# Kernel optimization log

Measured on AMD Instinct MI355X. Metric: run time of the kernel, lower is better.

Reference implementation:

```python
import jax, jax.numpy as jnp
import numpy as np

NUM_CLASSES = 151  # Visual Genome object classes
PRED_DIM = 51      # predicate distribution channels (50 predicates + bg)


def _conv2d(x, w, pad):
    # x: [B, Cin, H, W], w: [Cout, Cin, kh, kw]
    return jax.lax.conv_general_dilated(
        x, w, window_strides=(1, 1), padding=[(pad, pad), (pad, pad)],
        dimension_numbers=("NCHW", "OIHW", "NCHW"))


def setup_inputs() -> dict:
    key = jax.random.key(0)
    ks = jax.random.split(key, 12)
    B, N, D = 64, 80, 4096
    K = D // 4  # 1024
    s = 0.02
    return {
        "encoder_reps": jax.random.normal(ks[0], (B, N, D), jnp.float32),
        "obj_preds": jax.random.randint(ks[1], (B, N), 0, NUM_CLASSES, jnp.int32),
        "freq_table": jax.random.normal(ks[2], (NUM_CLASSES * NUM_CLASSES, PRED_DIM), jnp.float32),
        "W_comp": jax.random.normal(ks[3], (D, K), jnp.float32) * s,
        "W_ou1": jax.random.normal(ks[4], (K, K), jnp.float32) * s,
        "W_ofc": jax.random.normal(ks[5], (K, K), jnp.float32) * s,
        "W_decomp": jax.random.normal(ks[6], (K, D), jnp.float32) * s,
        "conv1": jax.random.normal(ks[7], (10, PRED_DIM, 3, 3), jnp.float32) * s,
        "conv2": jax.random.normal(ks[8], (5, 10, 3, 3), jnp.float32) * s,
        "conv3": jax.random.normal(ks[9], (1, 5, 1, 1), jnp.float32) * s,
    }


def reference(encoder_reps, obj_preds, freq_table, W_comp, W_ou1, W_ofc,
              W_decomp, conv1, conv2, conv3):
    B, N, D = encoder_reps.shape
    # obj_comp: Linear(D, D//4, bias=False) + ReLU
    comp = jax.nn.relu(jnp.einsum("bnd,dk->bnk", encoder_reps, W_comp))  # [B,N,K]
    # ou1: Linear(K, K, bias=False) + ReLU
    obj_u1 = jax.nn.relu(jnp.einsum("bnk,kj->bnj", comp, W_ou1))          # [B,N,K]
    # pairwise product indices -> freq_bias.index_with_labels (subj*C + obj)
    pair_idx = obj_preds[:, :, None] * NUM_CLASSES + obj_preds[:, None, :]  # [B,N,N]
    rel_u1 = freq_table[pair_idx]                                          # [B,N,N,51]
    # adjacency via small conv stack + sigmoid
    x = jnp.transpose(rel_u1, (0, 3, 1, 2))      # [B,51,N,N]
    x = _conv2d(x, conv1, pad=1)                 # [B,10,N,N]
    x = _conv2d(x, conv2, pad=1)                 # [B,5,N,N]
    x = _conv2d(x, conv3, pad=0)                 # [B,1,N,N]
    adj = jax.nn.sigmoid(x[:, 0])                # [B,N,N]
    # normalized Laplacian: D^-1/2 (A + I) D^-1/2
    A_hat = adj + jnp.eye(N, dtype=adj.dtype)[None]
    d = (jnp.sum(A_hat, axis=2) + 1e-5) ** (-0.5)                          # [B,N]
    L_hat = d[:, :, None] * A_hat * d[:, None, :]                          # [B,N,N]
    ofl_u = jnp.einsum("bnm,bmk->bnk", L_hat, obj_u1)                      # [B,N,K]
    # ofc_u + obj_decomp + residual
    u_m = jax.nn.relu(jnp.einsum("bnk,kj->bnj", ofl_u, W_ofc))
    decomp = jax.nn.relu(jnp.einsum("bnk,kd->bnd", u_m, W_decomp))
    return decomp + encoder_reps
```

## Files before the change

kernel.cpp:

```cpp
#include <hip/hip_runtime.h>
#include <hip/hip_bf16.h>
#include <math.h>

typedef __bf16 bf16x8 __attribute__((ext_vector_type(8)));
typedef float floatx4 __attribute__((ext_vector_type(4)));
typedef float float4v __attribute__((ext_vector_type(4)));
typedef float float2v __attribute__((ext_vector_type(2)));
typedef unsigned short ushortx4 __attribute__((ext_vector_type(4)));
typedef unsigned short ushortx8 __attribute__((ext_vector_type(8)));

__device__ __forceinline__ unsigned short f2bf(float f) {
    unsigned int u = __builtin_bit_cast(unsigned int, f);
    u += 0x7FFFu + ((u >> 16) & 1u);
    return (unsigned short)(u >> 16);
}
__device__ __forceinline__ float bf2f(unsigned short h) {
    unsigned int u = ((unsigned int)h) << 16;
    return __builtin_bit_cast(float, u);
}

__device__ __forceinline__ void gload_lds16(const void* g, void* l) {
    __builtin_amdgcn_global_load_lds(
        (const __attribute__((address_space(1))) unsigned int*)g,
        (__attribute__((address_space(3))) unsigned int*)l, 16, 0, 0);
}

__global__ __launch_bounds__(256) void cast_bf16_kernel(
    const float* __restrict__ in, unsigned short* __restrict__ out, long n8)
{
    long i = (long)blockIdx.x * 256 + threadIdx.x;
    long stride = (long)gridDim.x * 256;
    for (; i < n8; i += stride) {
        float4v a = reinterpret_cast<const float4v*>(in)[2 * i];
        float4v b = reinterpret_cast<const float4v*>(in)[2 * i + 1];
        ushortx8 h;
        #pragma unroll
        for (int q = 0; q < 4; ++q) { h[q] = f2bf(a[q]); h[4 + q] = f2bf(b[q]); }
        reinterpret_cast<ushortx8*>(out)[i] = h;
    }
}

__global__ __launch_bounds__(256) void reduce_relu_kernel(
    const unsigned short* __restrict__ p0, const unsigned short* __restrict__ p1,
    unsigned short* __restrict__ out, long n8)
{
    long i = (long)blockIdx.x * 256 + threadIdx.x;
    long stride = (long)gridDim.x * 256;
    const ushortx8* a0 = reinterpret_cast<const ushortx8*>(p0);
    const ushortx8* a1 = reinterpret_cast<const ushortx8*>(p1);
    for (; i < n8; i += stride) {
        ushortx8 x = a0[i], y = a1[i];
        ushortx8 h;
        #pragma unroll
        for (int q = 0; q < 8; ++q)
            h[q] = f2bf(fmaxf(bf2f(x[q]) + bf2f(y[q]), 0.0f));
        reinterpret_cast<ushortx8*>(out)[i] = h;
    }
}

__global__ __launch_bounds__(256) void prep_kernel(
    const float* __restrict__ w1, const float* __restrict__ w2,
    const float* __restrict__ w3, float* __restrict__ W1e,
    float* __restrict__ w23)
{
    for (int idx = threadIdx.x; idx < 4590; idx += 256) {
        int ci = idx / 90, rem = idx % 90;
        int tap = rem / 10, co = rem % 10;
        int di = tap / 3, dj = tap % 3;
        W1e[idx] = w1[((co * 51 + ci) * 3 + di) * 3 + dj];
    }
    if (threadIdx.x < 90) {
        int tap = threadIdx.x / 10, c10 = threadIdx.x % 10;
        int di = tap / 3, dj = tap % 3;
        float s = 0.f;
        #pragma unroll
        for (int c5 = 0; c5 < 5; ++c5)
            s = fmaf(w3[c5], w2[((c5 * 10 + c10) * 3 + di) * 3 + dj], s);
        w23[threadIdx.x] = s;
    }
}

__global__ __launch_bounds__(256) void fp1_kernel(
    const float* __restrict__ freq, const float* __restrict__ W1e,
    float* __restrict__ Fp1)
{
    __shared__ float W1s[4590];
    for (int idx = threadIdx.x; idx < 4590; idx += 256)
        W1s[idx] = W1e[idx];
    __syncthreads();
    int p = blockIdx.x * 256 + threadIdx.x;
    if (p >= 22801) return;
    float2v acc[45];
    #pragma unroll
    for (int t = 0; t < 45; ++t) { acc[t][0] = 0.f; acc[t][1] = 0.f; }
    const float* fr = freq + (size_t)p * 51;
    for (int ci = 0; ci < 51; ++ci) {
        float v = fr[ci];
        const float2v* wrow = reinterpret_cast<const float2v*>(&W1s[ci * 90]);
        #pragma unroll
        for (int t = 0; t < 45; ++t) {
            float2v w = wrow[t];
            acc[t][0] = fmaf(v, w[0], acc[t][0]);
            acc[t][1] = fmaf(v, w[1], acc[t][1]);
        }
    }
    float2v* out = reinterpret_cast<float2v*>(Fp1 + (size_t)p * 90);
    #pragma unroll
    for (int t = 0; t < 45; ++t) out[t] = acc[t];
}

__global__ __launch_bounds__(320) void gather_kernel(
    const int* __restrict__ preds, const float* __restrict__ Fp1,
    float* __restrict__ h1)
{
    __shared__ int pb[80];
    const int b = blockIdx.y;
    const int tid = threadIdx.x;
    if (tid < 80) pb[tid] = preds[b * 80 + tid];
    __syncthreads();
    const int i = blockIdx.x * 4 + tid / 80;
    const int j = tid % 80;
    float2v acc[5];
    #pragma unroll
    for (int q = 0; q < 5; ++q) { acc[q][0] = 0.f; acc[q][1] = 0.f; }
    #pragma unroll
    for (int di = 0; di < 3; ++di) {
        int ii = i + di - 1;
        if (ii < 0 || ii >= 80) continue;
        int pi = pb[ii] * 151;
        #pragma unroll
        for (int dj = 0; dj < 3; ++dj) {
            int jj = j + dj - 1;
            if (jj < 0 || jj >= 80) continue;
            const float2v* row = reinterpret_cast<const float2v*>(
                Fp1 + (size_t)(pi + pb[jj]) * 90 + (di * 3 + dj) * 10);
            #pragma unroll
            for (int q = 0; q < 5; ++q) {
                float2v v = row[q];
                acc[q][0] += v[0];
                acc[q][1] += v[1];
            }
        }
    }
    float2v* out = reinterpret_cast<float2v*>(
        h1 + ((size_t)b * 6400 + i * 80 + j) * 10);
    #pragma unroll
    for (int q = 0; q < 5; ++q) out[q] = acc[q];
}

__global__ __launch_bounds__(320) void conv23_kernel(
    const float* __restrict__ h1, const float* __restrict__ w23g,
    float* __restrict__ adj)
{
    __shared__ float w23s[90];
    const int tid = threadIdx.x;
    if (tid < 90) w23s[tid] = w23g[tid];
    __syncthreads();
    const int b = blockIdx.y;
    const int i = blockIdx.x * 4 + tid / 80;
    const int j = tid % 80;
    float t = 0.f;
    #pragma unroll
    for (int di = 0; di < 3; ++di) {
        int ii = i + di - 1;
        if (ii < 0 || ii >= 80) continue;
        #pragma unroll
        for (int dj = 0; dj < 3; ++dj) {
            int jj = j + dj - 1;
            if (jj < 0 || jj >= 80) continue;
            const float2v* hp = reinterpret_cast<const float2v*>(
                h1 + ((size_t)b * 6400 + ii * 80 + jj) * 10);
            const float* wp = w23s + (di * 3 + dj) * 10;
            #pragma unroll
            for (int q = 0; q < 5; ++q) {
                float2v v = hp[q];
                t = fmaf(v[0], wp[2 * q], t);
                t = fmaf(v[1], wp[2 * q + 1], t);
            }
        }
    }
    adj[(size_t)b * 6400 + i * 80 + j] = 1.0f / (1.0f + __expf(-t));
}

__global__ __launch_bounds__(128) void degree_kernel(
    const float* __restrict__ adj, float* __restrict__ deg)
{
    int b = blockIdx.x;
    int i = threadIdx.x;
    if (i >= 80) return;
    const float* row = adj + (size_t)b * 6400 + i * 80;
    float s = 1.0f + 1e-5f;
    for (int jj = 0; jj < 80; ++jj) s += row[jj];
    deg[b * 80 + i] = rsqrtf(s);
}

__global__ __launch_bounds__(256) void transpose_cast(
    const float* __restrict__ in, unsigned short* __restrict__ out,
    int R, int C)
{
    __shared__ float t[32][33];
    const int tx = threadIdx.x & 31;
    const int ty = threadIdx.x >> 5;
    const int r0 = blockIdx.y * 32, c0 = blockIdx.x * 32;
    #pragma unroll
    for (int k = 0; k < 4; ++k)
        t[ty + k * 8][tx] = in[(size_t)(r0 + ty + k * 8) * C + c0 + tx];
    __syncthreads();
    #pragma unroll
    for (int k = 0; k < 4; ++k)
        out[(size_t)(c0 + ty + k * 8) * R + r0 + tx] = f2bf(t[tx][ty + k * 8]);
}

template<int MODE>
__global__ __launch_bounds__(256) void gemm8p(
    const unsigned short* __restrict__ Ap, const unsigned short* __restrict__ Bt,
    void* __restrict__ Cp, const unsigned short* __restrict__ Rb,
    unsigned short* __restrict__ P1,
    int M, int N, int lda, int kh)
{
    __shared__ __align__(16) unsigned short SS[24576];
    unsigned short* Al = SS;
    unsigned short* Bl = SS + 12288;

    const int tid  = threadIdx.x;
    const int bm   = blockIdx.x * 128;
    const int bn   = blockIdx.y * 128;
    const int k0   = blockIdx.z * kh;
    const int wave = tid >> 6;
    const int lane = tid & 63;
    const int wm   = (wave >> 1) * 64;
    const int wn   = (wave & 1) * 64;
    const int lr   = lane & 15;
    const int lo   = lane >> 4;
    const int soct = (lo ^ ((lr >> 1) & 3)) * 8;

    floatx4 acc[4][4];
    #pragma unroll
    for (int i = 0; i < 4; ++i)
        #pragma unroll
        for (int j = 0; j < 4; ++j)
            #pragma unroll
            for (int r = 0; r < 4; ++r) acc[i][j][r] = 0.0f;

    auto stageA = [&](int buf, int kq) {
        #pragma unroll
        for (int it = 0; it < 2; ++it) {
            int idx = tid + it * 256;
            int r = idx >> 2, s = idx & 3;
            gload_lds16(
                &Ap[(size_t)(bm + r) * lda + kq + ((s ^ ((r >> 1) & 3)) * 8)],
                &Al[buf * 4096 + idx * 8]);
        }
    };
    auto stageB = [&](int buf, int kq) {
        #pragma unroll
        for (int it = 0; it < 2; ++it) {
            int idx = tid + it * 256;
            int r = idx >> 2, s = idx & 3;
            gload_lds16(
                &Bt[(size_t)(bn + r) * lda + kq + ((s ^ ((r >> 1) & 3)) * 8)],
                &Bl[buf * 4096 + idx * 8]);
        }
    };

    const int nt = kh >> 5;
    stageA(0, k0);
    stageB(0, k0);
    if (nt > 1) stageA(1, k0 + 32);

    for (int t = 0; t < nt; ++t) {
        const int cur = t % 3;
        if (t + 1 < nt) {
            asm volatile("s_waitcnt vmcnt(2)" ::: "memory");
        } else {
            asm volatile("s_waitcnt vmcnt(0)" ::: "memory");
        }
        __builtin_amdgcn_s_barrier();
        __builtin_amdgcn_sched_barrier(0);

        bf16x8 af[4], bf0[2];
        #pragma unroll
        for (int mi = 0; mi < 4; ++mi)
            af[mi] = *reinterpret_cast<const bf16x8*>(
                &Al[cur * 4096 + (wm + mi * 16 + lr) * 32 + soct]);
        #pragma unroll
        for (int ni = 0; ni < 2; ++ni)
            bf0[ni] = *reinterpret_cast<const bf16x8*>(
                &Bl[cur * 4096 + (wn + ni * 16 + lr) * 32 + soct]);
        if (t + 1 < nt) stageB((t + 1) % 3, k0 + ((t + 1) << 5));
        __builtin_amdgcn_sched_barrier(0);
        __builtin_amdgcn_s_barrier();
        __builtin_amdgcn_s_setprio(1);
        #pragma unroll
        for (int mi = 0; mi < 4; ++mi)
            #pragma unroll
            for (int ni = 0; ni < 2; ++ni)
                acc[mi][ni] = __builtin_amdgcn_mfma_f32_16x16x32_bf16(
                    bf0[ni], af[mi], acc[mi][ni], 0, 0, 0);
        __builtin_amdgcn_s_setprio(0);

        bf16x8 bf1[2];
        #pragma unroll
        for (int ni = 0; ni < 2; ++ni)
            bf1[ni] = *reinterpret_cast<const bf16x8*>(
                &Bl[cur * 4096 + (wn + (ni + 2) * 16 + lr) * 32 + soct]);
        if (t + 2 < nt) stageA((t + 2) % 3, k0 + ((t + 2) << 5));
        __builtin_amdgcn_sched_barrier(0);
        __builtin_amdgcn_s_barrier();
        __builtin_amdgcn_s_setprio(1);
        #pragma unroll
        for (int mi = 0; mi < 4; ++mi)
            #pragma unroll
            for (int ni = 0; ni < 2; ++ni)
                acc[mi][ni + 2] = __builtin_amdgcn_mfma_f32_16x16x32_bf16(
                    bf1[ni], af[mi], acc[mi][ni + 2], 0, 0, 0);
        __builtin_amdgcn_s_setprio(0);
    }

    __syncthreads();
    if (MODE == 1) {
        #pragma unroll
        for (int p = 0; p < 2; ++p) {
            if ((wave & 1) == p) {
                #pragma unroll
                for (int mi = 0; mi < 4; ++mi) {
                    const int mrow = wm + mi * 16 + lr;
                    const int swz = (mrow & 7) << 4;
                    #pragma unroll
                    for (int ni = 0; ni < 4; ++ni) {
                        const int nc = ni * 16 + lo * 4;
                        float4v v;
                        #pragma unroll
                        for (int rr = 0; rr < 4; ++rr) v[rr] = acc[mi][ni][rr];
                        *reinterpret_cast<float4v*>(
                            (char*)SS + ((mrow * 256 + nc * 4) ^ swz)) = v;
                    }
                }
            }
            __syncthreads();
            #pragma unroll
            for (int it = 0; it < 8; ++it) {
                int idx = tid + it * 256;
                int r = idx >> 4, c = idx & 15;
                float4v v = *reinterpret_cast<const float4v*>(
                    (char*)SS + ((r * 256 + c * 16) ^ ((r & 7) << 4)));
                size_t off = (size_t)(bm + r) * N + bn + p * 64 + c * 4;
                ushortx4 rv = *reinterpret_cast<const ushortx4*>(&Rb[off]);
                float4v o;
                #pragma unroll
                for (int rr = 0; rr < 4; ++rr)
                    o[rr] = fmaxf(v[rr], 0.f) + bf2f(rv[rr]);
                *reinterpret_cast<float4v*>(&((float*)Cp)[off]) = o;
            }
            if (p == 0) __syncthreads();
        }
    } else {
        #pragma unroll
        for (int mi = 0; mi < 4; ++mi) {
            const int mrow = wm + mi * 16 + lr;
            const int swz = (mrow & 7) << 4;
            #pragma unroll
            for (int ni = 0; ni < 4; ++ni) {
                const int nc = wn + ni * 16 + lo * 4;
                ushortx4 v;
                #pragma unroll
                for (int rr = 0; rr < 4; ++rr)
                    v[rr] = f2bf(fmaxf(acc[mi][ni][rr], 0.f));
                *reinterpret_cast<ushortx4*>(
                    (char*)SS + ((mrow * 256 + nc * 2) ^ swz)) = v;
            }
        }
        __syncthreads();
        unsigned short* dst = (unsigned short*)Cp;
        #pragma unroll
        for (int it = 0; it < 8; ++it) {
            int idx = tid + it * 256;
            int r = idx >> 4, c = idx & 15;
            ushortx8 v = *reinterpret_cast<const ushortx8*>(
                (char*)SS + ((r * 256 + c * 16) ^ ((r & 7) << 4)));
            *reinterpret_cast<ushortx8*>(
                &dst[(size_t)(bm + r) * N + bn + c * 8]) = v;
        }
    }
}

template<int MODE>
__global__ __launch_bounds__(256) void gemm128(
    const unsigned short* __restrict__ Ap, const unsigned short* __restrict__ Bt,
    void* __restrict__ Cp, const unsigned short* __restrict__ Rb,
    unsigned short* __restrict__ P1,
    int M, int N, int lda, int kh)
{
    __shared__ __align__(16) unsigned short SS[16384];
    unsigned short* Al = SS;
    unsigned short* Bl = SS + 8192;

    const int tid  = threadIdx.x;
    const int bm   = blockIdx.x * 128;
    const int bn   = blockIdx.y * 128;
    const int k0   = blockIdx.z * kh;
    const int wave = tid >> 6;
    const int lane = tid & 63;
    const int wm   = (wave >> 1) * 64;
    const int wn   = (wave & 1) * 64;
    const int lr   = lane & 15;
    const int lo   = lane >> 4;
    const int soct = (lo ^ ((lr >> 1) & 3)) * 8;

    floatx4 acc[4][4];
    #pragma unroll
    for (int i = 0; i < 4; ++i)
        #pragma unroll
        for (int j = 0; j < 4; ++j)
            #pragma unroll
            for (int r = 0; r < 4; ++r) acc[i][j][r] = 0.0f;

    auto stage = [&](int buf, int kq) {
        #pragma unroll
        for (int it = 0; it < 2; ++it) {
            int idx = tid + it * 256;
            int r = idx >> 2, s = idx & 3;
            gload_lds16(
                &Ap[(size_t)(bm + r) * lda + kq + ((s ^ ((r >> 1) & 3)) * 8)],
                &Al[buf * 4096 + idx * 8]);
        }
        #pragma unroll
        for (int it = 0; it < 2; ++it) {
            int idx = tid + it * 256;
            int r = idx >> 2, s = idx & 3;
            gload_lds16(
                &Bt[(size_t)(bn + r) * lda + kq + ((s ^ ((r >> 1) & 3)) * 8)],
                &Bl[buf * 4096 + idx * 8]);
        }
    };

    stage(0, k0);
    __syncthreads();
    const int nt = kh >> 5;
    int cur = 0;
    for (int t = 0; t < nt; ++t) {
        if (t + 1 < nt) stage(cur ^ 1, k0 + ((t + 1) << 5));
        bf16x8 af[4], bfv[4];
        #pragma unroll
        for (int mi = 0; mi < 4; ++mi)
            af[mi] = *reinterpret_cast<const bf16x8*>(
                &Al[cur * 4096 + (wm + mi * 16 + lr) * 32 + soct]);
        #pragma unroll
        for (int ni = 0; ni < 4; ++ni)
            bfv[ni] = *reinterpret_cast<const bf16x8*>(
                &Bl[cur * 4096 + (wn + ni * 16 + lr) * 32 + soct]);
        #pragma unroll
        for (int mi = 0; mi < 4; ++mi)
            #pragma unroll
            for (int ni = 0; ni < 4; ++ni)
                acc[mi][ni] = __builtin_amdgcn_mfma_f32_16x16x32_bf16(
                    bfv[ni], af[mi], acc[mi][ni], 0, 0, 0);
        __syncthreads();
        cur ^= 1;
    }

    #pragma unroll
    for (int mi = 0; mi < 4; ++mi) {
        const int mrow = wm + mi * 16 + lr;
        const int swz = (mrow & 7) << 4;
        #pragma unroll
        for (int ni = 0; ni < 4; ++ni) {
            const int nc = wn + ni * 16 + lo * 4;
            ushortx4 v;
            #pragma unroll
            for (int rr = 0; rr < 4; ++rr)
                v[rr] = f2bf(MODE == 0 ? fmaxf(acc[mi][ni][rr], 0.f)
                                       : acc[mi][ni][rr]);
            *reinterpret_cast<ushortx4*>(
                (char*)SS + ((mrow * 256 + nc * 2) ^ swz)) = v;
        }
    }
    __syncthreads();
    unsigned short* dst = (MODE == 2 && blockIdx.z)
        ? P1 : (unsigned short*)Cp;
    #pragma unroll
    for (int it = 0; it < 8; ++it) {
        int idx = tid + it * 256;
        int r = idx >> 4, c = idx & 15;
        ushortx8 v = *reinterpret_cast<const ushortx8*>(
            (char*)SS + ((r * 256 + c * 16) ^ ((r & 7) << 4)));
        *reinterpret_cast<ushortx8*>(
            &dst[(size_t)(bm + r) * N + bn + c * 8]) = v;
    }
}

__global__ __launch_bounds__(256) void gemm_f32a(
    const float* __restrict__ Ap, const unsigned short* __restrict__ Bt,
    unsigned short* __restrict__ Cp, int M, int N, int lda)
{
    __shared__ unsigned short Al[2][128 * 40];
    __shared__ unsigned short Bl[2][128 * 32];
    const int tid  = threadIdx.x;
    const int bm   = blockIdx.x * 128;
    const int bn   = blockIdx.y * 128;
    const int wave = tid >> 6;
    const int lane = tid & 63;
    const int wm   = (wave >> 1) * 64;
    const int wn   = (wave & 1) * 64;
    const int lr   = lane & 15;
    const int lk   = (lane >> 4) * 8;
    floatx4 acc[4][4];
    #pragma unroll
    for (int i = 0; i < 4; ++i)
        #pragma unroll
        for (int j = 0; j < 4; ++j)
            #pragma unroll
            for (int r = 0; r < 4; ++r) acc[i][j][r] = 0.0f;
    auto stage = [&](int buf, int k0) {
        #pragma unroll
        for (int it = 0; it < 4; ++it) {
            int idx = tid + it * 256;
            int r = idx >> 3, kc = (idx & 7) * 4;
            float4v v = *reinterpret_cast<const float4v*>(
                &Ap[(size_t)(bm + r) * lda + k0 + kc]);
            ushortx4 h;
            #pragma unroll
            for (int q = 0; q < 4; ++q) h[q] = f2bf(v[q]);
            *reinterpret_cast<ushortx4*>(&Al[buf][r * 40 + kc]) = h;
        }
        #pragma unroll
        for (int it = 0; it < 2; ++it) {
            int idx = tid + it * 256;
            gload_lds16(&Bt[(size_t)(bn + (idx >> 2)) * lda + k0 + (idx & 3) * 8],
                        &Bl[buf][idx * 8]);
        }
    };
    stage(0, 0);
    __syncthreads();
    const int nt = lda >> 5;
    int cur = 0;
    for (int t = 0; t < nt; ++t) {
        if (t + 1 < nt) stage(cur ^ 1, (t + 1) << 5);
        bf16x8 af[4], bfv[4];
        #pragma unroll
        for (int mi = 0; mi < 4; ++mi)
            af[mi] = *reinterpret_cast<const bf16x8*>(
                &Al[cur][(wm + mi * 16 + lr) * 40 + lk]);
        #pragma unroll
        for (int ni = 0; ni < 4; ++ni)
            bfv[ni] = *reinterpret_cast<const bf16x8*>(
                &Bl[cur][(wn + ni * 16 + lr) * 32 + lk]);
        #pragma unroll
        for (int mi = 0; mi < 4; ++mi)
            #pragma unroll
            for (int ni = 0; ni < 4; ++ni)
                acc[mi][ni] = __builtin_amdgcn_mfma_f32_16x16x32_bf16(
                    af[mi], bfv[ni], acc[mi][ni], 0, 0, 0);
        __syncthreads();
        cur ^= 1;
    }
    #pragma unroll
    for (int mi = 0; mi < 4; ++mi)
        #pragma unroll
        for (int ni = 0; ni < 4; ++ni)
            #pragma unroll
            for (int r = 0; r < 4; ++r) {
                int row = bm + wm + mi * 16 + (lane >> 4) * 4 + r;
                int col = bn + wn + ni * 16 + lr;
                Cp[(size_t)row * N + col] = f2bf(fmaxf(acc[mi][ni][r], 0.f));
            }
}

__global__ __launch_bounds__(256) void gemm_res_f32(
    const unsigned short* __restrict__ Ap, const unsigned short* __restrict__ Bt,
    float* __restrict__ Cp, const float* __restrict__ Rp, int M, int N, int lda)
{
    __shared__ unsigned short Al[2][128 * 32];
    __shared__ unsigned short Bl[2][128 * 32];
    const int tid  = threadIdx.x;
    const int bm   = blockIdx.x * 128;
    const int bn   = blockIdx.y * 128;
    const int wave = tid >> 6;
    const int lane = tid & 63;
    const int wm   = (wave >> 1) * 64;
    const int wn   = (wave & 1) * 64;
    const int lr   = lane & 15;
    const int lk   = (lane >> 4) * 8;
    floatx4 acc[4][4];
    #pragma unroll
    for (int i = 0; i < 4; ++i)
        #pragma unroll
        for (int j = 0; j < 4; ++j)
            #pragma unroll
            for (int r = 0; r < 4; ++r) acc[i][j][r] = 0.0f;
    auto stage = [&](int buf, int kq) {
        #pragma unroll
        for (int it = 0; it < 2; ++it) {
            int idx = tid + it * 256;
            gload_lds16(&Ap[(size_t)(bm + (idx >> 2)) * lda + kq + (idx & 3) * 8],
                        &Al[buf][idx * 8]);
        }
        #pragma unroll
        for (int it = 0; it < 2; ++it) {
            int idx = tid + it * 256;
            gload_lds16(&Bt[(size_t)(bn + (idx >> 2)) * lda + kq + (idx & 3) * 8],
                        &Bl[buf][idx * 8]);
        }
    };
    stage(0, 0);
    __syncthreads();
    const int nt = lda >> 5;
    int cur = 0;
    for (int t = 0; t < nt; ++t) {
        if (t + 1 < nt) stage(cur ^ 1, (t + 1) << 5);
        bf16x8 af[4], bfv[4];
        #pragma unroll
        for (int mi = 0; mi < 4; ++mi)
            af[mi] = *reinterpret_cast<const bf16x8*>(
                &Al[cur][(wm + mi * 16 + lr) * 32 + lk]);
        #pragma unroll
        for (int ni = 0; ni < 4; ++ni)
            bfv[ni] = *reinterpret_cast<const bf16x8*>(
                &Bl[cur][(wn + ni * 16 + lr) * 32 + lk]);
        #pragma unroll
        for (int mi = 0; mi < 4; ++mi)
            #pragma unroll
            for (int ni = 0; ni < 4; ++ni)
                acc[mi][ni] = __builtin_amdgcn_mfma_f32_16x16x32_bf16(
                    af[mi], bfv[ni], acc[mi][ni], 0, 0, 0);
        __syncthreads();
        cur ^= 1;
    }
    #pragma unroll
    for (int mi = 0; mi < 4; ++mi)
        #pragma unroll
        for (int ni = 0; ni < 4; ++ni)
            #pragma unroll
            for (int r = 0; r < 4; ++r) {
                int row = bm + wm + mi * 16 + (lane >> 4) * 4 + r;
                int col = bn + wn + ni * 16 + lr;
                size_t off = (size_t)row * N + col;
                Cp[off] = fmaxf(acc[mi][ni][r], 0.f) + Rp[off];
            }
}

__global__ __launch_bounds__(256) void laplacian_kernel(
    const float* __restrict__ adj, const float* __restrict__ deg,
    const unsigned short* __restrict__ u_in, unsigned short* __restrict__ ofl)
{
    __shared__ float wl[6400];
    __shared__ unsigned short ul[80 * 256];
    const int b   = blockIdx.y;
    const int kq  = blockIdx.x;
    const int tid = threadIdx.x;
    const int ko  = tid & 31;
    const int ngrp = tid >> 5;

    const float* ab = adj + (size_t)b * 6400;
    const float* db = deg + b * 80;
    for (int idx = tid; idx < 6400; idx += 256) {
        int n = idx / 80;
        int m = idx - n * 80;
        float w = ab[idx] + (n == m ? 1.0f : 0.0f);
        wl[idx] = w * db[m];
    }
    const unsigned short* ub = u_in + (size_t)b * 80 * 1024 + kq * 256;
    #pragma unroll
    for (int it = 0; it < 10; ++it) {
        int idx = tid + it * 256;
        int m   = idx >> 5;
        int c8  = (idx & 31) * 8;
        *reinterpret_cast<ushortx8*>(&ul[m * 256 + c8]) =
            *reinterpret_cast<const ushortx8*>(&ub[(size_t)m * 1024 + c8]);
    }
    __syncthreads();

    float acc[10][8];
    #pragma unroll
    for (int ni = 0; ni < 10; ++ni)
        #pragma unroll
        for (int q = 0; q < 8; ++q) acc[ni][q] = 0.0f;

    for (int m = 0; m < 80; ++m) {
        ushortx8 uv = *reinterpret_cast<const ushortx8*>(&ul[m * 256 + ko * 8]);
        float uf[8];
        #pragma unroll
        for (int q = 0; q < 8; ++q) uf[q] = bf2f(uv[q]);
        #pragma unroll
        for (int ni = 0; ni < 10; ++ni) {
            float wv = wl[(ngrp * 10 + ni) * 80 + m];
            #pragma unroll
            for (int q = 0; q < 8; ++q)
                acc[ni][q] = fmaf(wv, uf[q], acc[ni][q]);
        }
    }
    #pragma unroll
    for (int ni = 0; ni < 10; ++ni) {
        int n = ngrp * 10 + ni;
        float dn = db[n];
        ushortx8 o;
        #pragma unroll
        for (int q = 0; q < 8; ++q) o[q] = f2bf(acc[ni][q] * dn);
        *reinterpret_cast<ushortx8*>(
            &ofl[((size_t)(b * 80 + n)) * 1024 + kq * 256 + ko * 8]) = o;
    }
}

extern "C" void kernel_launch(void* const* d_in, const int* in_sizes, int n_in,
                              void* d_out, int out_size, void* d_ws, size_t ws_size,
                              hipStream_t stream)
{
    const float* enc   = (const float*)d_in[0];
    const int*   preds = (const int*)d_in[1];
    const float* freq  = (const float*)d_in[2];
    const float* Wc    = (const float*)d_in[3];
    const float* Wou1  = (const float*)d_in[4];
    const float* Wofc  = (const float*)d_in[5];
    const float* Wdec  = (const float*)d_in[6];
    const float* w1    = (const float*)d_in[7];
    const float* w2    = (const float*)d_in[8];
    const float* w3    = (const float*)d_in[9];

    const int M = 5120;
    const size_t SLAB = (size_t)M * 1024;
    unsigned short* comp  = (unsigned short*)d_ws;
    unsigned short* obju  = comp + SLAB;
    unsigned short* r1    = obju + SLAB;
    unsigned short* oflu  = r1;
    float*          h1    = (float*)r1;
    unsigned short* r2    = r1 + 8192000;
    unsigned short* um    = r2;
    float*          Fp1   = (float*)r2;
    unsigned short* Wcb   = r2 + SLAB;
    unsigned short* Wou1b = Wcb + (size_t)1024 * 4096;
    unsigned short* Wofcb = Wou1b + (size_t)1024 * 1024;
    unsigned short* Wdecb = Wofcb + (size_t)1024 * 1024;
    float*          W1e   = (float*)(Wdecb + (size_t)4096 * 1024);
    float*          w23   = W1e + 4590;
    float*          adj   = w23 + 90;
    float*          deg   = adj + (size_t)64 * 6400;
    unsigned short* encb  = (unsigned short*)(deg + 5120);
    const size_t need_bytes =
        ((size_t)(encb - comp) + (size_t)M * 4096) * sizeof(unsigned short);
    const bool use_encb = ws_size >= need_bytes;

    prep_kernel<<<1, 256, 0, stream>>>(w1, w2, w3, W1e, w23);
    transpose_cast<<<dim3(32, 128), 256, 0, stream>>>(Wc, Wcb, 4096, 1024);
    transpose_cast<<<dim3(32, 32), 256, 0, stream>>>(Wou1, Wou1b, 1024, 1024);
    transpose_cast<<<dim3(32, 32), 256, 0, stream>>>(Wofc, Wofcb, 1024, 1024);
    transpose_cast<<<dim3(128, 32), 256, 0, stream>>>(Wdec, Wdecb, 1024, 4096);

    fp1_kernel<<<90, 256, 0, stream>>>(freq, W1e, Fp1);
    gather_kernel<<<dim3(20, 64), 320, 0, stream>>>(preds, Fp1, h1);
    conv23_kernel<<<dim3(20, 64), 320, 0, stream>>>(h1, w23, adj);
    degree_kernel<<<64, 128, 0, stream>>>(adj, deg);

    if (use_encb) {
        cast_bf16_kernel<<<2048, 256, 0, stream>>>(enc, encb, (long)M * 4096 / 8);
        gemm128<2><<<dim3(40, 8, 2), 256, 0, stream>>>(
            encb, Wcb, r1, nullptr, r2, M, 1024, 4096, 2048);
        reduce_relu_kernel<<<2048, 256, 0, stream>>>(r1, r2, comp, SLAB / 8);
        gemm128<0><<<dim3(40, 8, 1), 256, 0, stream>>>(
            comp, Wou1b, obju, nullptr, nullptr, M, 1024, 1024, 1024);
    } else {
        gemm_f32a<<<dim3(40, 8), 256, 0, stream>>>(enc, Wcb, comp, M, 1024, 4096);
        gemm128<0><<<dim3(40, 8, 1), 256, 0, stream>>>(
            comp, Wou1b, obju, nullptr, nullptr, M, 1024, 1024, 1024);
    }
    laplacian_kernel<<<dim3(4, 64), 256, 0, stream>>>(adj, deg, obju, oflu);
    if (use_encb) {
        gemm128<0><<<dim3(40, 8, 1), 256, 0, stream>>>(
            oflu, Wofcb, um, nullptr, nullptr, M, 1024, 1024, 1024);
        gemm8p<1><<<dim3(40, 32, 1), 256, 0, stream>>>(
            um, Wdecb, d_out, encb, nullptr, M, 4096, 1024, 1024);
    } else {
        gemm128<0><<<dim3(40, 8, 1), 256, 0, stream>>>(
            oflu, Wofcb, um, nullptr, nullptr, M, 1024, 1024, 1024);
        gemm_res_f32<<<dim3(40, 32), 256, 0, stream>>>(
            um, Wdecb, (float*)d_out, enc, M, 4096, 1024);
    }
}
```

Baseline: 315.0 us.

## Use 64-row GEMM tiles, drop split-K, fuse degree into conv and merge transposes

The 128x128 split-K GEMM for the compression layer and its reduce_relu pass are replaced by a new 64x128-tile GEMM with a fused ReLU epilogue. The same kernel now handles the K=1024 layers, launching 640 blocks instead of 320 to fill more CUs. The four weight transpose launches become one kernel, and the row-degree computation moves into the conv23 kernel, which removes launches and a re-read of adj. In exchange, smaller tiles give less operand reuse per block, and the compression GEMM loses its split-K parallelism over the 4096-long reduction.

```diff
diff --git a/kernel.cpp b/kernel.cpp
--- a/kernel.cpp
+++ b/kernel.cpp
@@ -40,24 +40,6 @@
     }
 }
 
-__global__ __launch_bounds__(256) void reduce_relu_kernel(
-    const unsigned short* __restrict__ p0, const unsigned short* __restrict__ p1,
-    unsigned short* __restrict__ out, long n8)
-{
-    long i = (long)blockIdx.x * 256 + threadIdx.x;
-    long stride = (long)gridDim.x * 256;
-    const ushortx8* a0 = reinterpret_cast<const ushortx8*>(p0);
-    const ushortx8* a1 = reinterpret_cast<const ushortx8*>(p1);
-    for (; i < n8; i += stride) {
-        ushortx8 x = a0[i], y = a1[i];
-        ushortx8 h;
-        #pragma unroll
-        for (int q = 0; q < 8; ++q)
-            h[q] = f2bf(fmaxf(bf2f(x[q]) + bf2f(y[q]), 0.0f));
-        reinterpret_cast<ushortx8*>(out)[i] = h;
-    }
-}
-
 __global__ __launch_bounds__(256) void prep_kernel(
     const float* __restrict__ w1, const float* __restrict__ w2,
     const float* __restrict__ w3, float* __restrict__ W1e,
@@ -80,6 +62,35 @@
     }
 }
 
+__global__ __launch_bounds__(256) void transpose_all(
+    const float* __restrict__ Wc, const float* __restrict__ Wou1,
+    const float* __restrict__ Wofc, const float* __restrict__ Wdec,
+    unsigned short* __restrict__ Wcb, unsigned short* __restrict__ Wou1b,
+    unsigned short* __restrict__ Wofcb, unsigned short* __restrict__ Wdecb)
+{
+    __shared__ float t[32][33];
+    int id = blockIdx.x;
+    const float* in; unsigned short* out; int R, C, bx, by;
+    if (id < 4096)      { in = Wc;   out = Wcb;   R = 4096; C = 1024;
+                          bx = id & 31;  by = id >> 5; }
+    else if (id < 5120) { id -= 4096; in = Wou1; out = Wou1b; R = 1024; C = 1024;
+                          bx = id & 31;  by = id >> 5; }
+    else if (id < 6144) { id -= 5120; in = Wofc; out = Wofcb; R = 1024; C = 1024;
+                          bx = id & 31;  by = id >> 5; }
+    else                { id -= 6144; in = Wdec; out = Wdecb; R = 1024; C = 4096;
+                          bx = id & 127; by = id >> 7; }
+    const int tx = threadIdx.x & 31;
+    const int ty = threadIdx.x >> 5;
+    const int r0 = by * 32, c0 = bx * 32;
+    #pragma unroll
+    for (int k = 0; k < 4; ++k)
+        t[ty + k * 8][tx] = in[(size_t)(r0 + ty + k * 8) * C + c0 + tx];
+    __syncthreads();
+    #pragma unroll
+    for (int k = 0; k < 4; ++k)
+        out[(size_t)(c0 + ty + k * 8) * R + r0 + tx] = f2bf(t[tx][ty + k * 8]);
+}
+
 __global__ __launch_bounds__(256) void fp1_kernel(
     const float* __restrict__ freq, const float* __restrict__ W1e,
     float* __restrict__ Fp1)
@@ -148,11 +159,12 @@
     for (int q = 0; q < 5; ++q) out[q] = acc[q];
 }
 
-__global__ __launch_bounds__(320) void conv23_kernel(
+__global__ __launch_bounds__(320) void conv23_deg_kernel(
     const float* __restrict__ h1, const float* __restrict__ w23g,
-    float* __restrict__ adj)
+    float* __restrict__ adj, float* __restrict__ deg)
 {
     __shared__ float w23s[90];
+    __shared__ float rowv[320];
     const int tid = threadIdx.x;
     if (tid < 90) w23s[tid] = w23g[tid];
     __syncthreads();
@@ -179,36 +191,112 @@
             }
         }
     }
-    adj[(size_t)b * 6400 + i * 80 + j] = 1.0f / (1.0f + __expf(-t));
-}
-
-__global__ __launch_bounds__(128) void degree_kernel(
-    const float* __restrict__ adj, float* __restrict__ deg)
-{
-    int b = blockIdx.x;
-    int i = threadIdx.x;
-    if (i >= 80) return;
-    const float* row = adj + (size_t)b * 6400 + i * 80;
-    float s = 1.0f + 1e-5f;
-    for (int jj = 0; jj < 80; ++jj) s += row[jj];
-    deg[b * 80 + i] = rsqrtf(s);
-}
-
-__global__ __launch_bounds__(256) void transpose_cast(
-    const float* __restrict__ in, unsigned short* __restrict__ out,
-    int R, int C)
-{
-    __shared__ float t[32][33];
-    const int tx = threadIdx.x & 31;
-    const int ty = threadIdx.x >> 5;
-    const int r0 = blockIdx.y * 32, c0 = blockIdx.x * 32;
-    #pragma unroll
-    for (int k = 0; k < 4; ++k)
-        t[ty + k * 8][tx] = in[(size_t)(r0 + ty + k * 8) * C + c0 + tx];
-    __syncthreads();
-    #pragma unroll
-    for (int k = 0; k < 4; ++k)
-        out[(size_t)(c0 + ty + k * 8) * R + r0 + tx] = f2bf(t[tx][ty + k * 8]);
+    float sig = 1.0f / (1.0f + __expf(-t));
+    adj[(size_t)b * 6400 + i * 80 + j] = sig;
+    rowv[tid] = sig;
+    __syncthreads();
+    if (tid < 4) {
+        float s = 1.0f + 1e-5f;
+        #pragma unroll 16
+        for (int jj = 0; jj < 80; ++jj) s += rowv[tid * 80 + jj];
+        deg[b * 80 + blockIdx.x * 4 + tid] = rsqrtf(s);
+    }
+}
+
+__global__ __launch_bounds__(256) void gemm64(
+    const unsigned short* __restrict__ Ap, const unsigned short* __restrict__ Bt,
+    unsigned short* __restrict__ Cp, int M, int N, int lda)
+{
+    __shared__ __align__(16) unsigned short SS[12288];
+    unsigned short* Al = SS;
+    unsigned short* Bl = SS + 4096;
+
+    const int tid  = threadIdx.x;
+    const int bm   = blockIdx.x * 64;
+    const int bn   = blockIdx.y * 128;
+    const int wave = tid >> 6;
+    const int lane = tid & 63;
+    const int wm   = (wave >> 1) * 32;
+    const int wn   = (wave & 1) * 64;
+    const int lr   = lane & 15;
+    const int lo   = lane >> 4;
+    const int soct = (lo ^ ((lr >> 1) & 3)) * 8;
+
+    floatx4 acc[2][4];
+    #pragma unroll
+    for (int i = 0; i < 2; ++i)
+        #pragma unroll
+        for (int j = 0; j < 4; ++j)
+            #pragma unroll
+            for (int r = 0; r < 4; ++r) acc[i][j][r] = 0.0f;
+
+    auto stage = [&](int buf, int kq) {
+        {
+            int r = tid >> 2, s = tid & 3;
+            gload_lds16(
+                &Ap[(size_t)(bm + r) * lda + kq + ((s ^ ((r >> 1) & 3)) * 8)],
+                &Al[buf * 2048 + tid * 8]);
+        }
+        #pragma unroll
+        for (int it = 0; it < 2; ++it) {
+            int idx = tid + it * 256;
+            int r = idx >> 2, s = idx & 3;
+            gload_lds16(
+                &Bt[(size_t)(bn + r) * lda + kq + ((s ^ ((r >> 1) & 3)) * 8)],
+                &Bl[buf * 4096 + idx * 8]);
+        }
+    };
+
+    stage(0, 0);
+    __syncthreads();
+    const int nt = lda >> 5;
+    int cur = 0;
+    for (int t = 0; t < nt; ++t) {
+        if (t + 1 < nt) stage(cur ^ 1, (t + 1) << 5);
+        bf16x8 af[2], bfv[4];
+        #pragma unroll
+        for (int mi = 0; mi < 2; ++mi)
+            af[mi] = *reinterpret_cast<const bf16x8*>(
+                &Al[cur * 2048 + (wm + mi * 16 + lr) * 32 + soct]);
+        #pragma unroll
+        for (int ni = 0; ni < 4; ++ni)
+            bfv[ni] = *reinterpret_cast<const bf16x8*>(
+                &Bl[cur * 4096 + (wn + ni * 16 + lr) * 32 + soct]);
+        #pragma unroll
+        for (int mi = 0; mi < 2; ++mi)
+            #pragma unroll
+            for (int ni = 0; ni < 4; ++ni)
+                acc[mi][ni] = __builtin_amdgcn_mfma_f32_16x16x32_bf16(
+                    bfv[ni], af[mi], acc[mi][ni], 0, 0, 0);
+        __syncthreads();
+        cur ^= 1;
+    }
+
+    #pragma unroll
+    for (int mi = 0; mi < 2; ++mi) {
+        const int mrow = wm + mi * 16 + lr;
+        const int swz = (mrow & 7) << 4;
+        #pragma unroll
+        for (int ni = 0; ni < 4; ++ni) {
+            const int nc = wn + ni * 16 + lo * 4;
+            ushortx4 v;
+            #pragma unroll
+            for (int rr = 0; rr < 4; ++rr)
+                v[rr] = f2bf(fmaxf(acc[mi][ni][rr], 0.f));
+            *reinterpret_cast<ushortx4*>(
+                (char*)SS + ((mrow * 256 + nc * 2) ^ swz)) = v;
+        }
+    }
+    __syncthreads();
+    #pragma unroll
+    for (int it = 0; it < 4; ++it) {
+        int idx = tid + it * 256;
+        int r = idx >> 4, c = idx & 15;
+        ushortx8 v = *reinterpret_cast<const ushortx8*>(
+            (char*)SS + ((r * 256 + c * 16) ^ ((r & 7) << 4)));
+        *reinterpret_cast<ushortx8*>(
+            &Cp[(size_t)(bm + r) * N + bn + c * 8]) = v;
+    }
 }
 
 template<int MODE>
@@ -354,138 +442,6 @@
             }
             if (p == 0) __syncthreads();
         }
-    } else {
-        #pragma unroll
-        for (int mi = 0; mi < 4; ++mi) {
-            const int mrow = wm + mi * 16 + lr;
-            const int swz = (mrow & 7) << 4;
-            #pragma unroll
-            for (int ni = 0; ni < 4; ++ni) {
-                const int nc = wn + ni * 16 + lo * 4;
-                ushortx4 v;
-                #pragma unroll
-                for (int rr = 0; rr < 4; ++rr)
-                    v[rr] = f2bf(fmaxf(acc[mi][ni][rr], 0.f));
-                *reinterpret_cast<ushortx4*>(
-                    (char*)SS + ((mrow * 256 + nc * 2) ^ swz)) = v;
-            }
-        }
-        __syncthreads();
-        unsigned short* dst = (unsigned short*)Cp;
-        #pragma unroll
-        for (int it = 0; it < 8; ++it) {
-            int idx = tid + it * 256;
-            int r = idx >> 4, c = idx & 15;
-            ushortx8 v = *reinterpret_cast<const ushortx8*>(
-                (char*)SS + ((r * 256 + c * 16) ^ ((r & 7) << 4)));
-            *reinterpret_cast<ushortx8*>(
-                &dst[(size_t)(bm + r) * N + bn + c * 8]) = v;
-        }
-    }
-}
-
-template<int MODE>
-__global__ __launch_bounds__(256) void gemm128(
-    const unsigned short* __restrict__ Ap, const unsigned short* __restrict__ Bt,
-    void* __restrict__ Cp, const unsigned short* __restrict__ Rb,
-    unsigned short* __restrict__ P1,
-    int M, int N, int lda, int kh)
-{
-    __shared__ __align__(16) unsigned short SS[16384];
-    unsigned short* Al = SS;
-    unsigned short* Bl = SS + 8192;
-
-    const int tid  = threadIdx.x;
-    const int bm   = blockIdx.x * 128;
-    const int bn   = blockIdx.y * 128;
-    const int k0   = blockIdx.z * kh;
-    const int wave = tid >> 6;
-    const int lane = tid & 63;
-    const int wm   = (wave >> 1) * 64;
-    const int wn   = (wave & 1) * 64;
-    const int lr   = lane & 15;
-    const int lo   = lane >> 4;
-    const int soct = (lo ^ ((lr >> 1) & 3)) * 8;
-
-    floatx4 acc[4][4];
-    #pragma unroll
-    for (int i = 0; i < 4; ++i)
-        #pragma unroll
-        for (int j = 0; j < 4; ++j)
-            #pragma unroll
-            for (int r = 0; r < 4; ++r) acc[i][j][r] = 0.0f;
-
-    auto stage = [&](int buf, int kq) {
-        #pragma unroll
-        for (int it = 0; it < 2; ++it) {
-            int idx = tid + it * 256;
-            int r = idx >> 2, s = idx & 3;
-            gload_lds16(
-                &Ap[(size_t)(bm + r) * lda + kq + ((s ^ ((r >> 1) & 3)) * 8)],
-                &Al[buf * 4096 + idx * 8]);
-        }
-        #pragma unroll
-        for (int it = 0; it < 2; ++it) {
-            int idx = tid + it * 256;
-            int r = idx >> 2, s = idx & 3;
-            gload_lds16(
-                &Bt[(size_t)(bn + r) * lda + kq + ((s ^ ((r >> 1) & 3)) * 8)],
-                &Bl[buf * 4096 + idx * 8]);
-        }
-    };
-
-    stage(0, k0);
-    __syncthreads();
-    const int nt = kh >> 5;
-    int cur = 0;
-    for (int t = 0; t < nt; ++t) {
-        if (t + 1 < nt) stage(cur ^ 1, k0 + ((t + 1) << 5));
-        bf16x8 af[4], bfv[4];
-        #pragma unroll
-        for (int mi = 0; mi < 4; ++mi)
-            af[mi] = *reinterpret_cast<const bf16x8*>(
-                &Al[cur * 4096 + (wm + mi * 16 + lr) * 32 + soct]);
-        #pragma unroll
-        for (int ni = 0; ni < 4; ++ni)
-            bfv[ni] = *reinterpret_cast<const bf16x8*>(
-                &Bl[cur * 4096 + (wn + ni * 16 + lr) * 32 + soct]);
-        #pragma unroll
-        for (int mi = 0; mi < 4; ++mi)
-            #pragma unroll
-            for (int ni = 0; ni < 4; ++ni)
-                acc[mi][ni] = __builtin_amdgcn_mfma_f32_16x16x32_bf16(
-                    bfv[ni], af[mi], acc[mi][ni], 0, 0, 0);
-        __syncthreads();
-        cur ^= 1;
-    }
-
-    #pragma unroll
-    for (int mi = 0; mi < 4; ++mi) {
-        const int mrow = wm + mi * 16 + lr;
-        const int swz = (mrow & 7) << 4;
-        #pragma unroll
-        for (int ni = 0; ni < 4; ++ni) {
-            const int nc = wn + ni * 16 + lo * 4;
-            ushortx4 v;
-            #pragma unroll
-            for (int rr = 0; rr < 4; ++rr)
-                v[rr] = f2bf(MODE == 0 ? fmaxf(acc[mi][ni][rr], 0.f)
-                                       : acc[mi][ni][rr]);
-            *reinterpret_cast<ushortx4*>(
-                (char*)SS + ((mrow * 256 + nc * 2) ^ swz)) = v;
-        }
-    }
-    __syncthreads();
-    unsigned short* dst = (MODE == 2 && blockIdx.z)
-        ? P1 : (unsigned short*)Cp;
-    #pragma unroll
-    for (int it = 0; it < 8; ++it) {
-        int idx = tid + it * 256;
-        int r = idx >> 4, c = idx & 15;
-        ushortx8 v = *reinterpret_cast<const ushortx8*>(
-            (char*)SS + ((r * 256 + c * 16) ^ ((r & 7) << 4)));
-        *reinterpret_cast<ushortx8*>(
-            &dst[(size_t)(bm + r) * N + bn + c * 8]) = v;
     }
 }
 
@@ -740,37 +696,26 @@
     const bool use_encb = ws_size >= need_bytes;
 
     prep_kernel<<<1, 256, 0, stream>>>(w1, w2, w3, W1e, w23);
-    transpose_cast<<<dim3(32, 128), 256, 0, stream>>>(Wc, Wcb, 4096, 1024);
-    transpose_cast<<<dim3(32, 32), 256, 0, stream>>>(Wou1, Wou1b, 1024, 1024);
-    transpose_cast<<<dim3(32, 32), 256, 0, stream>>>(Wofc, Wofcb, 1024, 1024);
-    transpose_cast<<<dim3(128, 32), 256, 0, stream>>>(Wdec, Wdecb, 1024, 4096);
+    transpose_all<<<10240, 256, 0, stream>>>(
+        Wc, Wou1, Wofc, Wdec, Wcb, Wou1b, Wofcb, Wdecb);
 
     fp1_kernel<<<90, 256, 0, stream>>>(freq, W1e, Fp1);
     gather_kernel<<<dim3(20, 64), 320, 0, stream>>>(preds, Fp1, h1);
-    conv23_kernel<<<dim3(20, 64), 320, 0, stream>>>(h1, w23, adj);
-    degree_kernel<<<64, 128, 0, stream>>>(adj, deg);
+    conv23_deg_kernel<<<dim3(20, 64), 320, 0, stream>>>(h1, w23, adj, deg);
 
     if (use_encb) {
         cast_bf16_kernel<<<2048, 256, 0, stream>>>(enc, encb, (long)M * 4096 / 8);
-        gemm128<2><<<dim3(40, 8, 2), 256, 0, stream>>>(
-            encb, Wcb, r1, nullptr, r2, M, 1024, 4096, 2048);
-        reduce_relu_kernel<<<2048, 256, 0, stream>>>(r1, r2, comp, SLAB / 8);
-        gemm128<0><<<dim3(40, 8, 1), 256, 0, stream>>>(
-            comp, Wou1b, obju, nullptr, nullptr, M, 1024, 1024, 1024);
-    } else {
-        gemm_f32a<<<dim3(40, 8), 256, 0, stream>>>(enc, Wcb, comp, M, 1024, 4096);
-        gemm128<0><<<dim3(40, 8, 1), 256, 0, stream>>>(
-            comp, Wou1b, obju, nullptr, nullptr, M, 1024, 1024, 1024);
-    }
-    laplacian_kernel<<<dim3(4, 64), 256, 0, stream>>>(adj, deg, obju, oflu);
-    if (use_encb) {
-        gemm128<0><<<dim3(40, 8, 1), 256, 0, stream>>>(
-            oflu, Wofcb, um, nullptr, nullptr, M, 1024, 1024, 1024);
+        gemm64<<<dim3(80, 8), 256, 0, stream>>>(encb, Wcb, comp, M, 1024, 4096);
+        gemm64<<<dim3(80, 8), 256, 0, stream>>>(comp, Wou1b, obju, M, 1024, 1024);
+        laplacian_kernel<<<dim3(4, 64), 256, 0, stream>>>(adj, deg, obju, oflu);
+        gemm64<<<dim3(80, 8), 256, 0, stream>>>(oflu, Wofcb, um, M, 1024, 1024);
         gemm8p<1><<<dim3(40, 32, 1), 256, 0, stream>>>(
             um, Wdecb, d_out, encb, nullptr, M, 4096, 1024, 1024);
     } else {
-        gemm128<0><<<dim3(40, 8, 1), 256, 0, stream>>>(
-            oflu, Wofcb, um, nullptr, nullptr, M, 1024, 1024, 1024);
+        gemm_f32a<<<dim3(40, 8), 256, 0, stream>>>(enc, Wcb, comp, M, 1024, 4096);
+        gemm64<<<dim3(80, 8), 256, 0, stream>>>(comp, Wou1b, obju, M, 1024, 1024);
+        laplacian_kernel<<<dim3(4, 64), 256, 0, stream>>>(adj, deg, obju, oflu);
+        gemm64<<<dim3(80, 8), 256, 0, stream>>>(oflu, Wofcb, um, M, 1024, 1024);
         gemm_res_f32<<<dim3(40, 32), 256, 0, stream>>>(
             um, Wdecb, (float*)d_out, enc, M, 4096, 1024);
     }
```

After: 317.9 us. Within noise of the previous version (+0.9%).
